# Kernel optimization log

Hardware: AMD Instinct MI355X
Metric: run time of the kernel (lower is better)

The kernel has to match this reference:

```python
import jax, jax.numpy as jnp
import numpy as np

N = 4096      # batch size (PK-sampled)
D = 1024      # feature dim
K = 4         # instances per identity
NUM_IDS = N // K


def setup_inputs() -> dict:
    key = jax.random.key(0)
    inputs = jax.random.normal(key, (N, D), dtype=jnp.float32)
    # PK-structured labels: NUM_IDS identities, K instances each.
    targets = jnp.repeat(jnp.arange(NUM_IDS, dtype=jnp.int32), K)
    # Flags alternate within each identity -> every (same/diff id) x (same/diff flag)
    # combination is non-empty for every anchor row.
    flags = jnp.tile(jnp.array([0, 1, 0, 1], dtype=jnp.int32), N // 4)
    epoch = 10  # unused by the loss, kept for signature fidelity
    return {"inputs": inputs, "targets": targets, "flags": flags, "epoch": epoch}


def reference(inputs, targets, flags, epoch):
    # Pairwise Euclidean distances: ||a||^2 + ||b||^2 - 2 a.b, clamped + sqrt.
    sq = jnp.sum(inputs * inputs, axis=1, keepdims=True)          # [n,1]
    dist = sq + sq.T - 2.0 * (inputs @ inputs.T)                   # [n,n]
    dist = jnp.sqrt(jnp.clip(dist, 1e-12, None))

    same_id = targets[:, None] == targets[None, :]                 # mask_1
    same_fl = flags[:, None] == flags[None, :]                     # mask_2
    m_same_hp = same_id & same_fl
    m_same_hn = (~same_id) & same_fl
    m_dif_hp = same_id & (~same_fl)
    m_dif_hn = (~same_id) & (~same_fl)

    NEG = jnp.asarray(-jnp.inf, dist.dtype)
    POS = jnp.asarray(jnp.inf, dist.dtype)
    dist_same_ap = jnp.max(jnp.where(m_same_hp, dist, NEG), axis=1)
    dist_same_an = jnp.min(jnp.where(m_same_hn, dist, POS), axis=1)
    dist_dif_ap = jnp.max(jnp.where(m_dif_hp, dist, NEG), axis=1)
    dist_dif_an = jnp.min(jnp.where(m_dif_hn, dist, POS), axis=1)

    # torch: first index in the FULL row equal to the masked min (exact equality)
    same_min_idx = jnp.argmax(dist == dist_same_an[:, None], axis=1)  # [n]
    dif_min_idx = jnp.argmax(dist == dist_dif_an[:, None], axis=1)    # [n]
    dist_dif_neg = dist[same_min_idx, dif_min_idx]                    # [n]

    relu = jax.nn.relu
    # MarginRankingLoss(x1, x2, y=1) = mean(relu(x2 - x1 + margin))
    loss_same = jnp.mean(relu(dist_same_ap - dist_same_an + 0.8))
    loss_dif = jnp.mean(relu(dist_dif_ap - dist_dif_an + 0.5))
    loss_neg = jnp.mean(relu(dist_same_ap - dist_dif_neg + 0.3))
    return loss_same + loss_dif + loss_neg
```

## Files before the change

kernel.cpp:

```cpp
#include <hip/hip_runtime.h>

#define NROWS 4096
#define DIM   1024
#define NT    528

using f32x4 = __attribute__((ext_vector_type(4))) float;
using bfrag = __attribute__((ext_vector_type(8))) short;
typedef unsigned long long u64;

__device__ __forceinline__ unsigned short f2bf(float f) {
  unsigned u = __float_as_uint(f);
  u += 0x7fffu + ((u >> 16) & 1u);
  return (unsigned short)(u >> 16);
}
__device__ __forceinline__ float bf2f(unsigned short b) {
  return __uint_as_float(((unsigned)b) << 16);
}
__device__ __forceinline__ u64 shflx64(u64 v, int m) {
  int lo = __shfl_xor((int)(unsigned)(v & 0xffffffffull), m);
  int hi = __shfl_xor((int)(unsigned)(v >> 32), m);
  return ((u64)(unsigned)hi << 32) | (unsigned)lo;
}

__global__ void prep_kernel(const float* __restrict__ X, unsigned short* __restrict__ Xb,
                            float* __restrict__ sqv, float* out) {
  int row = blockIdx.x, t = threadIdx.x;
  float4 v = reinterpret_cast<const float4*>(X + (size_t)row * DIM)[t];
  unsigned short b0 = f2bf(v.x), b1 = f2bf(v.y), b2 = f2bf(v.z), b3 = f2bf(v.w);
  float f0 = bf2f(b0), f1 = bf2f(b1), f2 = bf2f(b2), f3 = bf2f(b3);
  float s = f0 * f0 + f1 * f1 + f2 * f2 + f3 * f3;
  reinterpret_cast<ushort4*>(Xb + (size_t)row * DIM)[t] = make_ushort4(b0, b1, b2, b3);
  for (int m = 32; m; m >>= 1) s += __shfl_xor(s, m);
  __shared__ float ws4[4];
  if ((t & 63) == 0) ws4[t >> 6] = s;
  __syncthreads();
  if (t == 0) {
    sqv[row] = (ws4[0] + ws4[1]) + (ws4[2] + ws4[3]);
    if (row == 0) out[0] = 0.f;
  }
}

#define STAGE(KS)                                                                \
  {                                                                              \
    _Pragma("unroll")                                                            \
    for (int qq = 0; qq < 4; ++qq) {                                             \
      int boff = (wave * 4 + qq) * 1024;                     \
      int r = (wave * 4 + qq) * 8 + (lane >> 3);        \
      const unsigned short* sA = Xb + (size_t)(row0 + r) * DIM + (KS) + ksrc;    \
      __builtin_amdgcn_global_load_lds(                                          \
          (const __attribute__((address_space(1))) void*)sA,                     \
          (__attribute__((address_space(3))) void*)(smem + boff), 16, 0, 0);     \
      const unsigned short* sB = Xb + (size_t)(col0 + r) * DIM + (KS) + ksrc;    \
      __builtin_amdgcn_global_load_lds(                                          \
          (const __attribute__((address_space(1))) void*)sB,                     \
          (__attribute__((address_space(3))) void*)(smem + 16384 + boff), 16, 0, 0); \
    }                                                                            \
  }

__global__ __launch_bounds__(256) void gram_kernel(
    const unsigned short* __restrict__ Xb, const float* __restrict__ sqv,
    const int* __restrict__ tg, const int* __restrict__ fl,
    float* __restrict__ PmS, float* __restrict__ PmD,
    u64* __restrict__ PnS, u64* __restrict__ PnD) {
  __shared__ __attribute__((aligned(16))) char smem[32768];
  __shared__ float srow[128], scol[128];
  __shared__ int rtagp[128], ctagp[128];

  int tm = 0, g = blockIdx.x, rem = 32;
  while (g >= rem) { g -= rem; rem--; tm++; }
  int tn = tm + g;
  const int row0 = tm * 128, col0 = tn * 128;
  const int tid = threadIdx.x;
  const int wave = tid >> 6, lane = tid & 63;
  const int q = lane >> 4, li = lane & 15;
  const int ksrc = ((lane & 7) ^ (lane >> 3)) * 8;

  if (tid < 128) {
    srow[tid] = sqv[row0 + tid];
    rtagp[tid] = (fl[row0 + tid] << 12) | tg[row0 + tid];
  } else {
    int c = tid - 128;
    scol[c] = sqv[col0 + c];
    ctagp[c] = (fl[col0 + c] << 12) | tg[col0 + c];
  }

  unsigned short (*As)[64] = (unsigned short (*)[64])smem;
  unsigned short (*Bs)[64] = (unsigned short (*)[64])(smem + 16384);

  f32x4 acc[4][4] = {};
  const int wr = (wave >> 1) * 64, wc = (wave & 1) * 64;

  for (int ks = 0; ks < DIM; ks += 64) {
    __syncthreads();
    STAGE(ks);
    __syncthreads();
#pragma unroll
    for (int kk = 0; kk < 2; ++kk) {
      bfrag a[4], b[4];
      int kel = ((kk * 4 + q) ^ (lane & 7)) * 8;
#pragma unroll
      for (int m = 0; m < 4; ++m)
        a[m] = *(const bfrag*)&As[wr + m * 16 + li][kel];
#pragma unroll
      for (int n = 0; n < 4; ++n)
        b[n] = *(const bfrag*)&Bs[wc + n * 16 + li][kel];
#pragma unroll
      for (int m = 0; m < 4; ++m)
#pragma unroll
        for (int n = 0; n < 4; ++n)
          acc[m][n] = __builtin_amdgcn_mfma_f32_16x16x32_bf16(a[m], b[n], acc[m][n], 0, 0, 0);
    }
  }
  __syncthreads();

  float* tab_mS = (float*)smem;
  float* tab_mD = (float*)(smem + 2048);
  u64*   tab_nS = (u64*)(smem + 4096);
  u64*   tab_nD = (u64*)(smem + 8192);

  float cmxS[4], cmxD[4];
  u64 cmnS[4], cmnD[4];
  int ctv[4]; float scv[4];
#pragma unroll
  for (int n = 0; n < 4; ++n) {
    cmxS[n] = -1.f; cmxD[n] = -1.f; cmnS[n] = ~0ull; cmnD[n] = ~0ull;
    int lc = wc + n * 16 + li; ctv[n] = ctagp[lc]; scv[n] = scol[lc];
  }
#pragma unroll
  for (int m = 0; m < 4; ++m)
#pragma unroll
    for (int r = 0; r < 4; ++r) {
      int lr = wr + m * 16 + q * 4 + r;
      int rt = rtagp[lr];
      float sr = srow[lr];
      u64 rbase = (unsigned)(row0 + lr);
      float rmxS = -1.f, rmxD = -1.f;
      u64 rmnS = ~0ull, rmnD = ~0ull;
#pragma unroll
      for (int n = 0; n < 4; ++n) {
        float d = sqrtf(fmaxf(sr + scv[n] - 2.0f * acc[m][n][r], 1e-12f));
        int x = rt ^ ctv[n];
        u64 db = (u64)__float_as_uint(d) << 32;
        u64 pkr = db | (unsigned)(col0 + wc + n * 16 + li);
        u64 pkc = db | rbase;
        if ((x & 0xFFF) == 0) {
          if ((x >> 12) == 0) { rmxS = fmaxf(rmxS, d); cmxS[n] = fmaxf(cmxS[n], d); }
          else                { rmxD = fmaxf(rmxD, d); cmxD[n] = fmaxf(cmxD[n], d); }
        } else {
          if ((x >> 12) == 0) { if (pkr < rmnS) rmnS = pkr; if (pkc < cmnS[n]) cmnS[n] = pkc; }
          else                { if (pkr < rmnD) rmnD = pkr; if (pkc < cmnD[n]) cmnD[n] = pkc; }
        }
      }
#pragma unroll
      for (int mk = 1; mk <= 8; mk <<= 1) {
        rmxS = fmaxf(rmxS, __shfl_xor(rmxS, mk));
        rmxD = fmaxf(rmxD, __shfl_xor(rmxD, mk));
        u64 o = shflx64(rmnS, mk); if (o < rmnS) rmnS = o;
        o = shflx64(rmnD, mk); if (o < rmnD) rmnD = o;
      }
      if (li == 0) {
        int slot = lr * 2 + (wave & 1);
        tab_mS[slot] = rmxS; tab_mD[slot] = rmxD;
        tab_nS[slot] = rmnS; tab_nD[slot] = rmnD;
      }
    }
#pragma unroll
  for (int n = 0; n < 4; ++n) {
#pragma unroll
    for (int mk = 16; mk <= 32; mk <<= 1) {
      cmxS[n] = fmaxf(cmxS[n], __shfl_xor(cmxS[n], mk));
      cmxD[n] = fmaxf(cmxD[n], __shfl_xor(cmxD[n], mk));
      u64 o = shflx64(cmnS[n], mk); if (o < cmnS[n]) cmnS[n] = o;
      o = shflx64(cmnD[n], mk); if (o < cmnD[n]) cmnD[n] = o;
    }
    if (lane < 16) {
      int lc = wc + n * 16 + lane;
      int slot = 256 + lc * 2 + (wave >> 1);
      tab_mS[slot] = cmxS[n]; tab_mD[slot] = cmxD[n];
      tab_nS[slot] = cmnS[n]; tab_nD[slot] = cmnD[n];
    }
  }
  __syncthreads();
  {
    int e = tid;
    float mS = fmaxf(tab_mS[2 * e], tab_mS[2 * e + 1]);
    float mD = fmaxf(tab_mD[2 * e], tab_mD[2 * e + 1]);
    u64 a = tab_nS[2 * e], b = tab_nS[2 * e + 1]; u64 nS = a < b ? a : b;
    a = tab_nD[2 * e]; b = tab_nD[2 * e + 1]; u64 nD = a < b ? a : b;
    size_t o = (size_t)blockIdx.x * 256 + e;
    PmS[o] = mS; PmD[o] = mD; PnS[o] = nS; PnD[o] = nD;
  }
}

__global__ void finstats_kernel(const float* __restrict__ PmS, const float* __restrict__ PmD,
                                const u64* __restrict__ PnS, const u64* __restrict__ PnD,
                                float* __restrict__ stP, float* __restrict__ stM,
                                int* __restrict__ stIA, int* __restrict__ stIB) {
  int r = blockIdx.x * 128 + threadIdx.x;
  int p = r >> 7, rl = r & 127;
  float mS = -1.f, mD = -1.f;
  u64 nS = ~0ull, nD = ~0ull;
  int g0 = p * 32 - (p * (p - 1)) / 2;
  for (int t = 0; t < 32 - p; ++t) {
    size_t base = (size_t)(g0 + t) * 256 + rl;
    mS = fmaxf(mS, PmS[base]); mD = fmaxf(mD, PmD[base]);
    u64 a = PnS[base]; if (a < nS) nS = a;
    u64 b = PnD[base]; if (b < nD) nD = b;
  }
  int gg = p;
  for (int t = 0; t <= p; ++t) {
    size_t base = (size_t)gg * 256 + 128 + rl;
    mS = fmaxf(mS, PmS[base]); mD = fmaxf(mD, PmD[base]);
    u64 a = PnS[base]; if (a < nS) nS = a;
    u64 b = PnD[base]; if (b < nD) nD = b;
    gg += 31 - t;
  }
  float mnSv = __uint_as_float((unsigned)(nS >> 32));
  float mnDv = __uint_as_float((unsigned)(nD >> 32));
  stP[r] = fmaxf(mS - mnSv + 0.8f, 0.f) + fmaxf(mD - mnDv + 0.5f, 0.f);
  stM[r] = mS;
  stIA[r] = (int)(nS & 0xffffffffull);
  stIB[r] = (int)(nD & 0xffffffffull);
}

__global__ void finloss_kernel(const unsigned short* __restrict__ Xb,
                               const float* __restrict__ sqv,
                               const float* __restrict__ stP, const float* __restrict__ stM,
                               const int* __restrict__ stIA, const int* __restrict__ stIB,
                               float* out) {
  int wave = threadIdx.x >> 6, lane = threadIdx.x & 63;
  float part = 0.f;
  for (int rr = 0; rr < 8; ++rr) {
    int row = blockIdx.x * 32 + wave * 8 + rr;
    int ia = stIA[row];
    int ib = stIB[row];
    const ushort4* pa = (const ushort4*)(Xb + (size_t)ia * DIM);
    const ushort4* pb = (const ushort4*)(Xb + (size_t)ib * DIM);
    float s = 0.f;
#pragma unroll
    for (int qq = 0; qq < 4; ++qq) {
      ushort4 a = pa[lane + qq * 64], b = pb[lane + qq * 64];
      s += bf2f(a.x) * bf2f(b.x) + bf2f(a.y) * bf2f(b.y) +
           bf2f(a.z) * bf2f(b.z) + bf2f(a.w) * bf2f(b.w);
    }
    for (int m = 32; m; m >>= 1) s += __shfl_xor(s, m);
    if (lane == 0) {
      float dneg = sqrtf(fmaxf(sqv[ia] + sqv[ib] - 2.f * s, 1e-12f));
      part += stP[row] + fmaxf(stM[row] - dneg + 0.3f, 0.f);
    }
  }
  __shared__ float wp[4];
  if (lane == 0) wp[wave] = part;
  __syncthreads();
  if (threadIdx.x == 0)
    atomicAdd(out, ((wp[0] + wp[1]) + (wp[2] + wp[3])) * (1.0f / 4096.0f));
}

extern "C" void kernel_launch(void* const* d_in, const int* in_sizes, int n_in,
                              void* d_out, int out_size, void* d_ws, size_t ws_size,
                              hipStream_t stream) {
  const float* X = (const float*)d_in[0];
  const int* tg  = (const int*)d_in[1];
  const int* fl  = (const int*)d_in[2];
  float* out = (float*)d_out;

  char* w = (char*)d_ws;
  unsigned short* Xb = (unsigned short*)(w);
  float* sqv = (float*)(w + 8388608);
  float* PmS = (float*)(w + 8404992);
  float* PmD = (float*)(w + 8945664);
  u64*   PnS = (u64*)(w + 9486336);
  u64*   PnD = (u64*)(w + 10567680);
  float* stP = (float*)(w + 11649024);
  float* stM = (float*)(w + 11665408);
  int*   stIA = (int*)(w + 11681792);
  int*   stIB = (int*)(w + 11698176);

  prep_kernel<<<NROWS, 256, 0, stream>>>(X, Xb, sqv, out);
  gram_kernel<<<NT, 256, 0, stream>>>(Xb, sqv, tg, fl, PmS, PmD, PnS, PnD);
  finstats_kernel<<<32, 128, 0, stream>>>(PmS, PmD, PnS, PnD, stP, stM, stIA, stIB);
  finloss_kernel<<<128, 256, 0, stream>>>(Xb, sqv, stP, stM, stIA, stIB, out);
}
```

Measured before the change: 164.3 us.

## Give each wave private LDS tiles to remove block-wide barriers in Gram loop

Each of the four waves now stages its own 64-row A and B slices into a private 16 KB LDS region and waits only on its own vmcnt. This replaces the shared block tile and drops both __syncthreads per k-step. The goal is to stop waves stalling on each other at barriers. In exchange, global-to-LDS traffic doubles because the row/column slices are loaded redundantly by two waves each, LDS use per block doubles to 64 KB (which can lower occupancy), and there is still no double buffering to hide load latency.

```diff
diff --git a/kernel.cpp b/kernel.cpp
--- a/kernel.cpp
+++ b/kernel.cpp
@@ -40,29 +40,12 @@
   }
 }
 
-#define STAGE(KS)                                                                \
-  {                                                                              \
-    _Pragma("unroll")                                                            \
-    for (int qq = 0; qq < 4; ++qq) {                                             \
-      int boff = (wave * 4 + qq) * 1024;                     \
-      int r = (wave * 4 + qq) * 8 + (lane >> 3);        \
-      const unsigned short* sA = Xb + (size_t)(row0 + r) * DIM + (KS) + ksrc;    \
-      __builtin_amdgcn_global_load_lds(                                          \
-          (const __attribute__((address_space(1))) void*)sA,                     \
-          (__attribute__((address_space(3))) void*)(smem + boff), 16, 0, 0);     \
-      const unsigned short* sB = Xb + (size_t)(col0 + r) * DIM + (KS) + ksrc;    \
-      __builtin_amdgcn_global_load_lds(                                          \
-          (const __attribute__((address_space(1))) void*)sB,                     \
-          (__attribute__((address_space(3))) void*)(smem + 16384 + boff), 16, 0, 0); \
-    }                                                                            \
-  }
-
 __global__ __launch_bounds__(256) void gram_kernel(
     const unsigned short* __restrict__ Xb, const float* __restrict__ sqv,
     const int* __restrict__ tg, const int* __restrict__ fl,
     float* __restrict__ PmS, float* __restrict__ PmD,
     u64* __restrict__ PnS, u64* __restrict__ PnD) {
-  __shared__ __attribute__((aligned(16))) char smem[32768];
+  __shared__ __attribute__((aligned(16))) char smem[65536];
   __shared__ float srow[128], scol[128];
   __shared__ int rtagp[128], ctagp[128];
 
@@ -84,26 +67,39 @@
     ctagp[c] = (fl[col0 + c] << 12) | tg[col0 + c];
   }
 
-  unsigned short (*As)[64] = (unsigned short (*)[64])smem;
-  unsigned short (*Bs)[64] = (unsigned short (*)[64])(smem + 16384);
+  const int wr = (wave >> 1) * 64, wc = (wave & 1) * 64;
+  char* wbase = smem + wave * 16384;
+  const int arow0 = row0 + wr, brow0 = col0 + wc;
+  unsigned short (*Aw)[64] = (unsigned short (*)[64])wbase;
+  unsigned short (*Bw)[64] = (unsigned short (*)[64])(wbase + 8192);
 
   f32x4 acc[4][4] = {};
-  const int wr = (wave >> 1) * 64, wc = (wave & 1) * 64;
 
   for (int ks = 0; ks < DIM; ks += 64) {
-    __syncthreads();
-    STAGE(ks);
-    __syncthreads();
+#pragma unroll
+    for (int j = 0; j < 8; ++j) {
+      int boff = j * 1024;
+      int ra = j * 8 + (lane >> 3);
+      const unsigned short* sA = Xb + (size_t)(arow0 + ra) * DIM + ks + ksrc;
+      __builtin_amdgcn_global_load_lds(
+          (const __attribute__((address_space(1))) void*)sA,
+          (__attribute__((address_space(3))) void*)(wbase + boff), 16, 0, 0);
+      const unsigned short* sB = Xb + (size_t)(brow0 + ra) * DIM + ks + ksrc;
+      __builtin_amdgcn_global_load_lds(
+          (const __attribute__((address_space(1))) void*)sB,
+          (__attribute__((address_space(3))) void*)(wbase + 8192 + boff), 16, 0, 0);
+    }
+    asm volatile("s_waitcnt vmcnt(0)" ::: "memory");
 #pragma unroll
     for (int kk = 0; kk < 2; ++kk) {
       bfrag a[4], b[4];
-      int kel = ((kk * 4 + q) ^ (lane & 7)) * 8;
+      int kel = ((kk * 4 + q) ^ (li & 7)) * 8;
 #pragma unroll
       for (int m = 0; m < 4; ++m)
-        a[m] = *(const bfrag*)&As[wr + m * 16 + li][kel];
+        a[m] = *(const bfrag*)&Aw[m * 16 + li][kel];
 #pragma unroll
       for (int n = 0; n < 4; ++n)
-        b[n] = *(const bfrag*)&Bs[wc + n * 16 + li][kel];
+        b[n] = *(const bfrag*)&Bw[n * 16 + li][kel];
 #pragma unroll
       for (int m = 0; m < 4; ++m)
 #pragma unroll
```

After: 166.2 us. Within noise of the previous version (+1.1%).

## Double-buffer gram tile loads with two waves per block and wider per-wave tiles

Applied to the files above, without the earlier changes.

Restructures the gram GEMM kernel to use 128 threads (2 waves) per block, each wave computing a 64x128 slice, with a BK=32 double-buffered LDS pipeline that issues the next K-slab's global-to-LDS loads while the current slab is being multiplied. It replaces the two full syncthreads per 64-wide K step with vmcnt/lgkmcnt waits and raw barriers. The epilogue is adjusted for the new wave-to-tile mapping. The aim is to hide global load latency behind MFMA work. In exchange the per-wave accumulator count doubles, raising register pressure, and there are fewer waves per block to hide latency.

```diff
diff --git a/kernel.cpp b/kernel.cpp
--- a/kernel.cpp
+++ b/kernel.cpp
@@ -40,24 +40,40 @@
   }
 }
 
-#define STAGE(KS)                                                                \
+#define STAGE(BASE, KS)                                                          \
   {                                                                              \
     _Pragma("unroll")                                                            \
-    for (int qq = 0; qq < 4; ++qq) {                                             \
-      int boff = (wave * 4 + qq) * 1024;                     \
-      int r = (wave * 4 + qq) * 8 + (lane >> 3);        \
-      const unsigned short* sA = Xb + (size_t)(row0 + r) * DIM + (KS) + ksrc;    \
+    for (int jj = 0; jj < 4; ++jj) {                                             \
+      int ch = wave * 4 + jj;                              \
+      int boff = ch * 1024;                                                      \
+      int rr = ch * 16 + (lane >> 2);                   \
+      const unsigned short* sA = Xb + (size_t)(row0 + rr) * DIM + (KS) + ksrc;   \
       __builtin_amdgcn_global_load_lds(                                          \
           (const __attribute__((address_space(1))) void*)sA,                     \
-          (__attribute__((address_space(3))) void*)(smem + boff), 16, 0, 0);     \
-      const unsigned short* sB = Xb + (size_t)(col0 + r) * DIM + (KS) + ksrc;    \
+          (__attribute__((address_space(3))) void*)((BASE) + boff), 16, 0, 0);   \
+      const unsigned short* sB = Xb + (size_t)(col0 + rr) * DIM + (KS) + ksrc;   \
       __builtin_amdgcn_global_load_lds(                                          \
           (const __attribute__((address_space(1))) void*)sB,                     \
-          (__attribute__((address_space(3))) void*)(smem + 16384 + boff), 16, 0, 0); \
+          (__attribute__((address_space(3))) void*)((BASE) + 8192 + boff), 16, 0, 0); \
     }                                                                            \
   }
 
-__global__ __launch_bounds__(256) void gram_kernel(
+#define BODY(BASE)                                                              \
+  {                                                                             \
+    unsigned short(*As_)[32] = (unsigned short(*)[32])(BASE);                   \
+    unsigned short(*Bs_)[32] = (unsigned short(*)[32])((BASE) + 8192);          \
+    bfrag a[4], b[8];                                                           \
+    int kel = (q ^ (li & 3)) * 8;                                               \
+    _Pragma("unroll") for (int m = 0; m < 4; ++m)                               \
+      a[m] = *(const bfrag*)&As_[wr + m * 16 + li][kel];                        \
+    _Pragma("unroll") for (int n = 0; n < 8; ++n)                               \
+      b[n] = *(const bfrag*)&Bs_[n * 16 + li][kel];                             \
+    _Pragma("unroll") for (int m = 0; m < 4; ++m)                               \
+      _Pragma("unroll") for (int n = 0; n < 8; ++n)                             \
+        acc[m][n] = __builtin_amdgcn_mfma_f32_16x16x32_bf16(a[m], b[n], acc[m][n], 0, 0, 0); \
+  }
+
+__global__ __launch_bounds__(128, 2) void gram_kernel(
     const unsigned short* __restrict__ Xb, const float* __restrict__ sqv,
     const int* __restrict__ tg, const int* __restrict__ fl,
     float* __restrict__ PmS, float* __restrict__ PmD,
@@ -73,44 +89,34 @@
   const int tid = threadIdx.x;
   const int wave = tid >> 6, lane = tid & 63;
   const int q = lane >> 4, li = lane & 15;
-  const int ksrc = ((lane & 7) ^ (lane >> 3)) * 8;
-
-  if (tid < 128) {
-    srow[tid] = sqv[row0 + tid];
-    rtagp[tid] = (fl[row0 + tid] << 12) | tg[row0 + tid];
-  } else {
-    int c = tid - 128;
-    scol[c] = sqv[col0 + c];
-    ctagp[c] = (fl[col0 + c] << 12) | tg[col0 + c];
-  }
-
-  unsigned short (*As)[64] = (unsigned short (*)[64])smem;
-  unsigned short (*Bs)[64] = (unsigned short (*)[64])(smem + 16384);
-
-  f32x4 acc[4][4] = {};
-  const int wr = (wave >> 1) * 64, wc = (wave & 1) * 64;
-
-  for (int ks = 0; ks < DIM; ks += 64) {
-    __syncthreads();
-    STAGE(ks);
-    __syncthreads();
-#pragma unroll
-    for (int kk = 0; kk < 2; ++kk) {
-      bfrag a[4], b[4];
-      int kel = ((kk * 4 + q) ^ (lane & 7)) * 8;
-#pragma unroll
-      for (int m = 0; m < 4; ++m)
-        a[m] = *(const bfrag*)&As[wr + m * 16 + li][kel];
-#pragma unroll
-      for (int n = 0; n < 4; ++n)
-        b[n] = *(const bfrag*)&Bs[wc + n * 16 + li][kel];
-#pragma unroll
-      for (int m = 0; m < 4; ++m)
-#pragma unroll
-        for (int n = 0; n < 4; ++n)
-          acc[m][n] = __builtin_amdgcn_mfma_f32_16x16x32_bf16(a[m], b[n], acc[m][n], 0, 0, 0);
-    }
-  }
+  const int ksrc = ((lane & 3) ^ ((lane >> 2) & 3)) * 8;
+
+  char* B0 = smem;
+  char* B1 = smem + 16384;
+
+  STAGE(B0, 0);
+  STAGE(B1, 32);
+  srow[tid] = sqv[row0 + tid];
+  rtagp[tid] = (fl[row0 + tid] << 12) | tg[row0 + tid];
+  scol[tid] = sqv[col0 + tid];
+  ctagp[tid] = (fl[col0 + tid] << 12) | tg[col0 + tid];
+
+  const int wr = wave * 64;
+  f32x4 acc[4][8] = {};
+
+  for (int tt = 0; tt < 31; ++tt) {
+    asm volatile("s_waitcnt vmcnt(8)" ::: "memory");
+    __builtin_amdgcn_s_barrier();
+    if (tt & 1) { BODY(B1); } else { BODY(B0); }
+    asm volatile("s_waitcnt lgkmcnt(0)" ::: "memory");
+    __builtin_amdgcn_s_barrier();
+    if (tt < 30) {
+      if (tt & 1) { STAGE(B1, (tt + 2) * 32); } else { STAGE(B0, (tt + 2) * 32); }
+    }
+  }
+  asm volatile("s_waitcnt vmcnt(0)" ::: "memory");
+  __builtin_amdgcn_s_barrier();
+  BODY(B1);
   __syncthreads();
 
   float* tab_mS = (float*)smem;
@@ -118,13 +124,13 @@
   u64*   tab_nS = (u64*)(smem + 4096);
   u64*   tab_nD = (u64*)(smem + 8192);
 
-  float cmxS[4], cmxD[4];
-  u64 cmnS[4], cmnD[4];
-  int ctv[4]; float scv[4];
-#pragma unroll
-  for (int n = 0; n < 4; ++n) {
+  float cmxS[8], cmxD[8];
+  u64 cmnS[8], cmnD[8];
+  int ctv[8]; float scv[8];
+#pragma unroll
+  for (int n = 0; n < 8; ++n) {
     cmxS[n] = -1.f; cmxD[n] = -1.f; cmnS[n] = ~0ull; cmnD[n] = ~0ull;
-    int lc = wc + n * 16 + li; ctv[n] = ctagp[lc]; scv[n] = scol[lc];
+    int lc = n * 16 + li; ctv[n] = ctagp[lc]; scv[n] = scol[lc];
   }
 #pragma unroll
   for (int m = 0; m < 4; ++m)
@@ -137,11 +143,11 @@
       float rmxS = -1.f, rmxD = -1.f;
       u64 rmnS = ~0ull, rmnD = ~0ull;
 #pragma unroll
-      for (int n = 0; n < 4; ++n) {
+      for (int n = 0; n < 8; ++n) {
         float d = sqrtf(fmaxf(sr + scv[n] - 2.0f * acc[m][n][r], 1e-12f));
         int x = rt ^ ctv[n];
         u64 db = (u64)__float_as_uint(d) << 32;
-        u64 pkr = db | (unsigned)(col0 + wc + n * 16 + li);
+        u64 pkr = db | (unsigned)(col0 + n * 16 + li);
         u64 pkc = db | rbase;
         if ((x & 0xFFF) == 0) {
           if ((x >> 12) == 0) { rmxS = fmaxf(rmxS, d); cmxS[n] = fmaxf(cmxS[n], d); }
@@ -159,13 +165,12 @@
         o = shflx64(rmnD, mk); if (o < rmnD) rmnD = o;
       }
       if (li == 0) {
-        int slot = lr * 2 + (wave & 1);
-        tab_mS[slot] = rmxS; tab_mD[slot] = rmxD;
-        tab_nS[slot] = rmnS; tab_nD[slot] = rmnD;
+        tab_mS[lr] = rmxS; tab_mD[lr] = rmxD;
+        tab_nS[lr] = rmnS; tab_nD[lr] = rmnD;
       }
     }
 #pragma unroll
-  for (int n = 0; n < 4; ++n) {
+  for (int n = 0; n < 8; ++n) {
 #pragma unroll
     for (int mk = 16; mk <= 32; mk <<= 1) {
       cmxS[n] = fmaxf(cmxS[n], __shfl_xor(cmxS[n], mk));
@@ -174,21 +179,23 @@
       o = shflx64(cmnD[n], mk); if (o < cmnD[n]) cmnD[n] = o;
     }
     if (lane < 16) {
-      int lc = wc + n * 16 + lane;
-      int slot = 256 + lc * 2 + (wave >> 1);
+      int lc = n * 16 + lane;
+      int slot = 128 + lc * 2 + wave;
       tab_mS[slot] = cmxS[n]; tab_mD[slot] = cmxD[n];
       tab_nS[slot] = cmnS[n]; tab_nD[slot] = cmnD[n];
     }
   }
   __syncthreads();
   {
-    int e = tid;
-    float mS = fmaxf(tab_mS[2 * e], tab_mS[2 * e + 1]);
-    float mD = fmaxf(tab_mD[2 * e], tab_mD[2 * e + 1]);
-    u64 a = tab_nS[2 * e], b = tab_nS[2 * e + 1]; u64 nS = a < b ? a : b;
-    a = tab_nD[2 * e]; b = tab_nD[2 * e + 1]; u64 nD = a < b ? a : b;
-    size_t o = (size_t)blockIdx.x * 256 + e;
-    PmS[o] = mS; PmD[o] = mD; PnS[o] = nS; PnD[o] = nD;
+    size_t ob = (size_t)blockIdx.x * 256;
+    PmS[ob + tid] = tab_mS[tid]; PmD[ob + tid] = tab_mD[tid];
+    PnS[ob + tid] = tab_nS[tid]; PnD[ob + tid] = tab_nD[tid];
+    float mS = fmaxf(tab_mS[128 + tid * 2], tab_mS[128 + tid * 2 + 1]);
+    float mD = fmaxf(tab_mD[128 + tid * 2], tab_mD[128 + tid * 2 + 1]);
+    u64 a = tab_nS[128 + tid * 2], b = tab_nS[128 + tid * 2 + 1]; u64 nS = a < b ? a : b;
+    a = tab_nD[128 + tid * 2]; b = tab_nD[128 + tid * 2 + 1]; u64 nD = a < b ? a : b;
+    PmS[ob + 128 + tid] = mS; PmD[ob + 128 + tid] = mD;
+    PnS[ob + 128 + tid] = nS; PnD[ob + 128 + tid] = nD;
   }
 }
 
@@ -277,7 +284,7 @@
   int*   stIB = (int*)(w + 11698176);
 
   prep_kernel<<<NROWS, 256, 0, stream>>>(X, Xb, sqv, out);
-  gram_kernel<<<NT, 256, 0, stream>>>(Xb, sqv, tg, fl, PmS, PmD, PnS, PnD);
+  gram_kernel<<<NT, 128, 0, stream>>>(Xb, sqv, tg, fl, PmS, PmD, PnS, PnD);
   finstats_kernel<<<32, 128, 0, stream>>>(PmS, PmD, PnS, PnD, stP, stM, stIA, stIB);
   finloss_kernel<<<128, 256, 0, stream>>>(Xb, sqv, stP, stM, stIA, stIB, out);
 }
```

Result: slower. 245.0 us (+49.1%).
